# Optimization experiments

Hardware: AMD Instinct MI355X
Metric: run time of the kernel (lower is better)

## Reference

```python
import jax, jax.numpy as jnp
import numpy as np


def setup_inputs() -> dict:
    key = jax.random.key(0)
    k1, k2, k3, k4 = jax.random.split(key, 4)
    N, M, D = 4096, 4096, 1024
    H = jax.random.normal(k1, (N, D), dtype=jnp.float32)
    K = jax.random.normal(k2, (M, D), dtype=jnp.float32)
    V = jax.random.normal(k3, (M, D), dtype=jnp.float32)
    attn_mask = jax.random.uniform(k4, (N, M), dtype=jnp.float32)
    return {"H": H, "K": K, "V": V, "attn_mask": attn_mask}


def reference(H, K, V, attn_mask):
    # scores: [N, M] = H @ K^T, scaled by sqrt(d)
    d = H.shape[1]
    scores = jnp.matmul(H, K.T) / jnp.sqrt(jnp.asarray(d, dtype=H.dtype))
    # double softmax with elementwise mask multiply in between
    probs = jax.nn.softmax(jax.nn.softmax(scores, axis=1) * attn_mask, axis=1)
    return jnp.matmul(probs, V)
```

## Files before the change

kernel.cpp:

```cpp
#include <hip/hip_runtime.h>
#include <cstdint>

typedef unsigned short u16;
typedef __bf16 bf16x8 __attribute__((ext_vector_type(8)));
typedef float f32x4 __attribute__((ext_vector_type(4)));
typedef unsigned int u32x4 __attribute__((ext_vector_type(4)));

__device__ __forceinline__ float bf2f(u16 h) {
  union { unsigned int u; float f; } v; v.u = ((unsigned int)h) << 16; return v.f;
}
__device__ __forceinline__ u16 f2bf(float f) {
  union { float f; unsigned int u; } v; v.f = f;
  unsigned int u = v.u;
  return (u16)((u + 0x7FFFu + ((u >> 16) & 1u)) >> 16);
}

__device__ __forceinline__ void ld_lds16(const void* g, void* l) {
  __builtin_amdgcn_global_load_lds(
      (const __attribute__((address_space(1))) unsigned int*)g,
      (__attribute__((address_space(3))) unsigned int*)l, 16, 0, 0);
}

__global__ __launch_bounds__(512, 2) void gemm1_kernel(
    const u16* __restrict__ A, const u16* __restrict__ B,
    u16* __restrict__ S, int ldA, int ldB, int ldC)
{
  __shared__ __align__(16) u16 smem[65536];

  const int tid  = threadIdx.x;
  const int lane = tid & 63;
  const int w    = tid >> 6;
  const int wr   = w >> 2;
  const int wc   = w & 3;
  const int quad = lane >> 4;
  const int cIn  = lane & 15;
  const int lrow   = lane >> 3;
  const int gchunk = (lane & 7) ^ lrow;

  const int flat = blockIdx.x;
  const int xcd  = flat & 7;
  const int i    = flat >> 3;
  const int rowT = (xcd >> 1) * 4 + (i & 3);
  const int colT = (xcd & 1) * 8 + (i >> 2);
  const int rowBlk = rowT * 256;
  const int colBlk = colT * 256;

  f32x4 acc[8][4];
  #pragma unroll
  for (int a = 0; a < 8; ++a)
    #pragma unroll
    for (int b = 0; b < 4; ++b) acc[a][b] = {0.f, 0.f, 0.f, 0.f};

  auto stageA = [&](int buf, int kt2) {
    #pragma unroll
    for (int l = 0; l < 4; ++l) {
      const u16* ga = A + (size_t)(rowBlk + l * 64 + w * 8 + lrow) * ldA
                        + kt2 * 64 + gchunk * 8;
      ld_lds16(ga, &smem[buf * 16384 + l * 4096 + w * 512]);
    }
  };
  auto stageB = [&](int buf, int kt2) {
    #pragma unroll
    for (int l = 0; l < 4; ++l) {
      const u16* gb = B + (size_t)(colBlk + l * 64 + w * 8 + lrow) * ldB
                        + kt2 * 64 + gchunk * 8;
      ld_lds16(gb, &smem[32768 + buf * 16384 + l * 4096 + w * 512]);
    }
  };

  stageA(0, 0);
  stageB(0, 0);
  stageA(1, 1);
  stageB(1, 1);

  for (int kt = 0; kt < 16; ++kt) {
    const int cur = kt & 1;
    const int aBase = cur * 16384;
    const int bBase = 32768 + cur * 16384;

    if (kt < 15) asm volatile("s_waitcnt vmcnt(8)" ::: "memory");
    else         asm volatile("s_waitcnt vmcnt(0)" ::: "memory");
    __builtin_amdgcn_s_barrier();
    __builtin_amdgcn_sched_barrier(0);

    bf16x8 bf[4][2];
    #pragma unroll
    for (int q = 0; q < 4; ++q) {
      if (q == 0) {
        #pragma unroll
        for (int ni = 0; ni < 4; ++ni)
          #pragma unroll
          for (int ks = 0; ks < 2; ++ks) {
            int row = wc * 64 + ni * 16 + cIn;
            int ch  = (ks * 4 + quad) ^ (row & 7);
            bf[ni][ks] = *(const bf16x8*)&smem[bBase + row * 64 + ch * 8];
          }
      }

      bf16x8 af[2][2];
      #pragma unroll
      for (int m = 0; m < 2; ++m)
        #pragma unroll
        for (int ks = 0; ks < 2; ++ks) {
          int row = wr * 128 + (q * 2 + m) * 16 + cIn;
          int ch  = (ks * 4 + quad) ^ (row & 7);
          af[m][ks] = *(const bf16x8*)&smem[aBase + row * 64 + ch * 8];
        }

      __builtin_amdgcn_s_barrier();
      asm volatile("s_waitcnt lgkmcnt(0)" ::: "memory");
      __builtin_amdgcn_sched_barrier(0);
      __builtin_amdgcn_s_setprio(1);
      #pragma unroll
      for (int m = 0; m < 2; ++m)
        #pragma unroll
        for (int ni = 0; ni < 4; ++ni)
          #pragma unroll
          for (int ks = 0; ks < 2; ++ks)
            acc[q * 2 + m][ni] = __builtin_amdgcn_mfma_f32_16x16x32_bf16(
                af[m][ks], bf[ni][ks], acc[q * 2 + m][ni], 0, 0, 0);
      __builtin_amdgcn_s_setprio(0);
      __builtin_amdgcn_sched_barrier(0);
      __builtin_amdgcn_s_barrier();
    }

    if (kt + 2 < 16) {
      stageA(cur, kt + 2);
      stageB(cur, kt + 2);
    }
  }

  const float scale = 0.03125f;
  u16* epi = smem;
  #pragma unroll
  for (int R = 0; R < 2; ++R) {
    #pragma unroll
    for (int m2 = 0; m2 < 4; ++m2) {
      int mi = R * 4 + m2;
      #pragma unroll
      for (int ni = 0; ni < 4; ++ni) {
        int col = wc * 64 + ni * 16 + cIn;
        #pragma unroll
        for (int r = 0; r < 4; ++r) {
          int er = wr * 64 + m2 * 16 + quad * 4 + r;
          epi[er * 264 + col] = f2bf(acc[mi][ni][r] * scale);
        }
      }
    }
    __syncthreads();
    #pragma unroll
    for (int it = 0; it < 8; ++it) {
      int idx = it * 512 + tid;
      int er  = idx >> 5;
      int c8  = idx & 31;
      int grow = rowBlk + (er >> 6) * 128 + R * 64 + (er & 63);
      u32x4 v = *(const u32x4*)&epi[er * 264 + c8 * 8];
      *(u32x4*)&S[(size_t)grow * ldC + colBlk + c8 * 8] = v;
    }
    __syncthreads();
  }
}

__global__ __launch_bounds__(512, 2) void gemm2_kernel(
    const u16* __restrict__ A, const u16* __restrict__ B,
    float* __restrict__ Out, const float* __restrict__ L2,
    int ldA, int ldB, int ldC)
{
  __shared__ __align__(16) u16 smem[49152];

  const int tid  = threadIdx.x;
  const int lane = tid & 63;
  const int w    = tid >> 6;
  const int wk   = w & 1;
  const int wrow = (w >> 1) & 1;
  const int wcol = (w >> 2) & 1;
  const int quad = lane >> 4;
  const int cIn  = lane & 15;
  const int lrow   = lane >> 3;
  const int gchunk = (lane & 7) ^ lrow;

  const int flat = blockIdx.x;
  const int xcd  = flat & 7;
  const int i    = flat >> 3;
  const int rowBlk = (xcd * 4 + (i & 3)) * 128;
  const int colBlk = (i >> 2) * 128;

  f32x4 acc[4][4];
  #pragma unroll
  for (int a = 0; a < 4; ++a)
    #pragma unroll
    for (int b = 0; b < 4; ++b) acc[a][b] = {0.f, 0.f, 0.f, 0.f};

  auto stage = [&](int buf, int kt) {
    int kk = kt * 64;
    #pragma unroll
    for (int t = 0; t < 2; ++t) {
      int rg = w * 2 + t;
      const u16* ga = A + (size_t)(rowBlk + rg * 8 + lrow) * ldA + kk + gchunk * 8;
      ld_lds16(ga, &smem[buf * 8192 + rg * 512]);
      const u16* gb = B + (size_t)(colBlk + rg * 8 + lrow) * ldB + kk + gchunk * 8;
      ld_lds16(gb, &smem[24576 + buf * 8192 + rg * 512]);
    }
  };

  stage(0, 0);
  stage(1, 1);

  int cur = 0;
  for (int kt = 0; kt < 64; ++kt) {
    if (kt < 63) asm volatile("s_waitcnt vmcnt(4)" ::: "memory");
    else         asm volatile("s_waitcnt vmcnt(0)" ::: "memory");
    __builtin_amdgcn_s_barrier();
    __builtin_amdgcn_sched_barrier(0);

    if (kt + 2 < 64) {
      int nb = cur + 2; if (nb >= 3) nb -= 3;
      stage(nb, kt + 2);
    }

    const int aBase = cur * 8192;
    const int bBase = 24576 + cur * 8192;
    bf16x8 af[4], bfr[4];
    #pragma unroll
    for (int mi = 0; mi < 4; ++mi) {
      int row = wrow * 64 + mi * 16 + cIn;
      int ch  = (wk * 4 + quad) ^ (row & 7);
      af[mi]  = *(const bf16x8*)&smem[aBase + row * 64 + ch * 8];
    }
    #pragma unroll
    for (int ni = 0; ni < 4; ++ni) {
      int row = wcol * 64 + ni * 16 + cIn;
      int ch  = (wk * 4 + quad) ^ (row & 7);
      bfr[ni] = *(const bf16x8*)&smem[bBase + row * 64 + ch * 8];
    }
    __builtin_amdgcn_s_setprio(1);
    #pragma unroll
    for (int mi = 0; mi < 4; ++mi)
      #pragma unroll
      for (int ni = 0; ni < 4; ++ni)
        acc[mi][ni] = __builtin_amdgcn_mfma_f32_16x16x32_bf16(
            af[mi], bfr[ni], acc[mi][ni], 0, 0, 0);
    __builtin_amdgcn_s_setprio(0);

    cur = (cur + 1 == 3) ? 0 : cur + 1;
  }

  float* red = (float*)smem;
  const int ow = w >> 1;
  const int rbase = ow * 4160 + lane * 65;
  __syncthreads();
  if (wk == 1) {
    #pragma unroll
    for (int mi = 0; mi < 4; ++mi)
      #pragma unroll
      for (int ni = 0; ni < 4; ++ni)
        #pragma unroll
        for (int r = 0; r < 4; ++r)
          red[rbase + (mi * 4 + ni) * 4 + r] = acc[mi][ni][r];
  }
  __syncthreads();
  if (wk == 0) {
    #pragma unroll
    for (int mi = 0; mi < 4; ++mi) {
      #pragma unroll
      for (int r = 0; r < 4; ++r) {
        int row   = rowBlk + wrow * 64 + mi * 16 + quad * 4 + r;
        float inv = 1.0f / L2[row];
        #pragma unroll
        for (int ni = 0; ni < 4; ++ni) {
          int col = colBlk + wcol * 64 + ni * 16 + cIn;
          float v = acc[mi][ni][r] + red[rbase + (mi * 4 + ni) * 4 + r];
          __builtin_nontemporal_store(v * inv, &Out[(size_t)row * ldC + col]);
        }
      }
    }
  }
}

__global__ __launch_bounds__(256) void prep_kernel(
    const float* __restrict__ H, const float* __restrict__ Kin,
    const float* __restrict__ V, u16* __restrict__ Hb, u16* __restrict__ Kb,
    u16* __restrict__ Vt)
{
  int b = blockIdx.x;
  if (b < 8192) {
    const float* src = (b < 4096) ? H : Kin;
    u16* dst = (b < 4096) ? Hb : Kb;
    int i = (b & 4095) * 256 + threadIdx.x;
    f32x4 v = __builtin_nontemporal_load(&((const f32x4*)src)[i]);
    ushort4 o;
    o.x = f2bf(v.x); o.y = f2bf(v.y); o.z = f2bf(v.z); o.w = f2bf(v.w);
    ((ushort4*)dst)[i] = o;
  } else {
    __shared__ float tile[32][33];
    b -= 8192;
    int c0 = (b & 31) * 32;
    int r0 = (b >> 5) * 32;
    int tx = threadIdx.x & 31, ty = threadIdx.x >> 5;
    #pragma unroll
    for (int s = 0; s < 32; s += 8)
      tile[ty + s][tx] = __builtin_nontemporal_load(
          &V[(size_t)(r0 + ty + s) * 1024 + c0 + tx]);
    __syncthreads();
    #pragma unroll
    for (int s = 0; s < 32; s += 8)
      Vt[(size_t)(c0 + ty + s) * 4096 + r0 + tx] = f2bf(tile[tx][ty + s]);
  }
}

__global__ __launch_bounds__(256) void softmax2_kernel(
    u16* __restrict__ S, const float* __restrict__ mask,
    float* __restrict__ L2, int M)
{
  int row = blockIdx.x;
  u16* srow = S + (size_t)row * M;
  const float* mrow = mask + (size_t)row * M;
  const int base = threadIdx.x * 16;

  u16 sl[16];
  *(uint4*)(sl)     = *(const uint4*)(srow + base);
  *(uint4*)(sl + 8) = *(const uint4*)(srow + base + 8);

  float e[16];
  float s1 = 0.f;
  #pragma unroll
  for (int j = 0; j < 16; ++j) { e[j] = __expf(bf2f(sl[j])); s1 += e[j]; }

  __shared__ float wred[8];
  #pragma unroll
  for (int m = 1; m < 64; m <<= 1) s1 += __shfl_xor(s1, m, 64);
  if ((threadIdx.x & 63) == 0) wred[threadIdx.x >> 6] = s1;
  __syncthreads();
  float inv = 1.0f / (wred[0] + wred[1] + wred[2] + wred[3]);

  float mv[16];
  #pragma unroll
  for (int q = 0; q < 4; ++q) {
    f32x4 m4 = __builtin_nontemporal_load((const f32x4*)(mrow + base + q * 4));
    mv[q * 4 + 0] = m4.x; mv[q * 4 + 1] = m4.y;
    mv[q * 4 + 2] = m4.z; mv[q * 4 + 3] = m4.w;
  }

  float lsum = 0.f;
  #pragma unroll
  for (int j = 0; j < 16; ++j) {
    float p = __expf(e[j] * inv * mv[j]);
    lsum += p;
    sl[j] = f2bf(p);
  }
  *(uint4*)(srow + base)     = *(uint4*)(sl);
  *(uint4*)(srow + base + 8) = *(uint4*)(sl + 8);

  #pragma unroll
  for (int m = 1; m < 64; m <<= 1) lsum += __shfl_xor(lsum, m, 64);
  if ((threadIdx.x & 63) == 0) wred[4 + (threadIdx.x >> 6)] = lsum;
  __syncthreads();
  if (threadIdx.x == 0) L2[row] = wred[4] + wred[5] + wred[6] + wred[7];
}

extern "C" void kernel_launch(void* const* d_in, const int* in_sizes, int n_in,
                              void* d_out, int out_size, void* d_ws, size_t ws_size,
                              hipStream_t stream) {
  const float* H    = (const float*)d_in[0];
  const float* Kin  = (const float*)d_in[1];
  const float* V    = (const float*)d_in[2];
  const float* mask = (const float*)d_in[3];
  float* out = (float*)d_out;

  const int N = 4096, M = 4096, D = 1024;

  char* ws = (char*)d_ws;
  u16*   Hb = (u16*)(ws);
  u16*   Kb = (u16*)(ws + (8ull << 20));
  u16*   Vt = (u16*)(ws + (16ull << 20));
  u16*   S  = (u16*)(ws + (24ull << 20));
  float* L2 = (float*)(ws + (56ull << 20));

  prep_kernel<<<dim3(12288), dim3(256), 0, stream>>>(H, Kin, V, Hb, Kb, Vt);

  gemm1_kernel<<<dim3(256), dim3(512), 0, stream>>>(Hb, Kb, S, D, D, M);

  softmax2_kernel<<<dim3(N), dim3(256), 0, stream>>>(S, mask, L2, M);

  gemm2_kernel<<<dim3(256), dim3(512), 0, stream>>>(S, Vt, out, L2, M, M, D);
}
```

Before: 229.6 us.

## Double-buffer A fragments across MFMA sub-steps and vectorize V transpose stores

In the GEMM1 inner loop, B fragments and the first A fragments are now loaded before the q loop. The next sub-step's A fragments are prefetched into an alternate register set while the current MFMAs run, and the explicit lgkmcnt wait and per-substep trailing barrier are removed. This is meant to hide LDS read latency behind matrix math, at the cost of more VGPRs, which may pressure occupancy at launch bounds 512x2. Separately, the V transpose/convert path now writes 16-byte packed bf16 stores from 128 threads instead of scalar 2-byte stores from all threads.

```diff
diff --git a/kernel.cpp b/kernel.cpp
--- a/kernel.cpp
+++ b/kernel.cpp
@@ -85,44 +85,57 @@
 
     bf16x8 bf[4][2];
     #pragma unroll
+    for (int ni = 0; ni < 4; ++ni)
+      #pragma unroll
+      for (int ks = 0; ks < 2; ++ks) {
+        int row = wc * 64 + ni * 16 + cIn;
+        int ch  = (ks * 4 + quad) ^ (row & 7);
+        bf[ni][ks] = *(const bf16x8*)&smem[bBase + row * 64 + ch * 8];
+      }
+    bf16x8 afA[2][2], afB[2][2];
+    #pragma unroll
+    for (int m = 0; m < 2; ++m)
+      #pragma unroll
+      for (int ks = 0; ks < 2; ++ks) {
+        int row = wr * 128 + m * 16 + cIn;
+        int ch  = (ks * 4 + quad) ^ (row & 7);
+        afA[m][ks] = *(const bf16x8*)&smem[aBase + row * 64 + ch * 8];
+      }
+
+    #pragma unroll
     for (int q = 0; q < 4; ++q) {
-      if (q == 0) {
+      if (q < 3) {
+        #pragma unroll
+        for (int m = 0; m < 2; ++m)
+          #pragma unroll
+          for (int ks = 0; ks < 2; ++ks) {
+            int row = wr * 128 + ((q + 1) * 2 + m) * 16 + cIn;
+            int ch  = (ks * 4 + quad) ^ (row & 7);
+            bf16x8 v = *(const bf16x8*)&smem[aBase + row * 64 + ch * 8];
+            if (q & 1) afA[m][ks] = v; else afB[m][ks] = v;
+          }
+      }
+      __builtin_amdgcn_sched_barrier(0);
+      __builtin_amdgcn_s_barrier();
+      __builtin_amdgcn_sched_barrier(0);
+      __builtin_amdgcn_s_setprio(1);
+      #pragma unroll
+      for (int m = 0; m < 2; ++m)
         #pragma unroll
         for (int ni = 0; ni < 4; ++ni)
           #pragma unroll
           for (int ks = 0; ks < 2; ++ks) {
-            int row = wc * 64 + ni * 16 + cIn;
-            int ch  = (ks * 4 + quad) ^ (row & 7);
-            bf[ni][ks] = *(const bf16x8*)&smem[bBase + row * 64 + ch * 8];
+            if (q & 1)
+              acc[q * 2 + m][ni] = __builtin_amdgcn_mfma_f32_16x16x32_bf16(
+                  afB[m][ks], bf[ni][ks], acc[q * 2 + m][ni], 0, 0, 0);
+            else
+              acc[q * 2 + m][ni] = __builtin_amdgcn_mfma_f32_16x16x32_bf16(
+                  afA[m][ks], bf[ni][ks], acc[q * 2 + m][ni], 0, 0, 0);
           }
-      }
-
-      bf16x8 af[2][2];
-      #pragma unroll
-      for (int m = 0; m < 2; ++m)
-        #pragma unroll
-        for (int ks = 0; ks < 2; ++ks) {
-          int row = wr * 128 + (q * 2 + m) * 16 + cIn;
-          int ch  = (ks * 4 + quad) ^ (row & 7);
-          af[m][ks] = *(const bf16x8*)&smem[aBase + row * 64 + ch * 8];
-        }
-
-      __builtin_amdgcn_s_barrier();
-      asm volatile("s_waitcnt lgkmcnt(0)" ::: "memory");
-      __builtin_amdgcn_sched_barrier(0);
-      __builtin_amdgcn_s_setprio(1);
-      #pragma unroll
-      for (int m = 0; m < 2; ++m)
-        #pragma unroll
-        for (int ni = 0; ni < 4; ++ni)
-          #pragma unroll
-          for (int ks = 0; ks < 2; ++ks)
-            acc[q * 2 + m][ni] = __builtin_amdgcn_mfma_f32_16x16x32_bf16(
-                af[m][ks], bf[ni][ks], acc[q * 2 + m][ni], 0, 0, 0);
       __builtin_amdgcn_s_setprio(0);
       __builtin_amdgcn_sched_barrier(0);
-      __builtin_amdgcn_s_barrier();
-    }
+    }
+    __builtin_amdgcn_s_barrier();
 
     if (kt + 2 < 16) {
       stageA(cur, kt + 2);
@@ -302,9 +315,18 @@
       tile[ty + s][tx] = __builtin_nontemporal_load(
           &V[(size_t)(r0 + ty + s) * 1024 + c0 + tx]);
     __syncthreads();
-    #pragma unroll
-    for (int s = 0; s < 32; s += 8)
-      Vt[(size_t)(c0 + ty + s) * 4096 + r0 + tx] = f2bf(tile[tx][ty + s]);
+    if (threadIdx.x < 128) {
+      int vr = threadIdx.x >> 2;
+      int ch = threadIdx.x & 3;
+      u32x4 ov;
+      #pragma unroll
+      for (int p = 0; p < 4; ++p) {
+        unsigned int lo = f2bf(tile[ch * 8 + p * 2][vr]);
+        unsigned int hi = f2bf(tile[ch * 8 + p * 2 + 1][vr]);
+        ov[p] = lo | (hi << 16);
+      }
+      *(u32x4*)&Vt[(size_t)(c0 + vr) * 4096 + r0 + ch * 8] = ov;
+    }
   }
 }
 
```

New measurement: 228.1 us. Within noise of the previous version (-0.7%).
